# Optimization experiments

Hardware: AMD Instinct MI355X
Metric: run time of the kernel (lower is better)

Reference implementation:

```python
import jax, jax.numpy as jnp
import numpy as np

NUM_Q = 50000
DIM_KEY = 128
DIM_VALUE = 256
DIM_HIDDEN = 512
MEM_SIZE = 50
BATCH = 128
SEQ = 2048


def setup_inputs() -> dict:
    key = jax.random.key(0)
    ks = jax.random.split(key, 12)
    inp = {
        "q": jax.random.randint(ks[0], (BATCH, SEQ), 0, NUM_Q + 1, dtype=jnp.int64 if jax.config.jax_enable_x64 else jnp.int32),
        "a": jax.random.randint(ks[1], (BATCH, SEQ), 0, 2, dtype=jnp.int64 if jax.config.jax_enable_x64 else jnp.int32),
        # learned parameters (torch Linear convention: y = x @ W.T + b)
        "key_memory": jax.random.normal(ks[2], (MEM_SIZE, DIM_KEY), jnp.float32) * 0.1,
        "value_memory": jax.random.normal(ks[3], (MEM_SIZE, DIM_VALUE), jnp.float32) * 0.1,
        "embed_table": jax.random.normal(ks[4], (NUM_Q + 1, DIM_KEY), jnp.float32) * 0.1,
        "W_erase": jax.random.normal(ks[5], (DIM_VALUE, DIM_HIDDEN), jnp.float32) * 0.05,
        "b_erase": jnp.zeros((DIM_VALUE,), jnp.float32),
        "W_add": jax.random.normal(ks[6], (DIM_VALUE, DIM_HIDDEN), jnp.float32) * 0.05,
        "b_add": jnp.zeros((DIM_VALUE,), jnp.float32),
        "W_f": jax.random.normal(ks[7], (DIM_HIDDEN, DIM_VALUE + DIM_KEY), jnp.float32) * 0.05,
        "b_f": jnp.zeros((DIM_HIDDEN,), jnp.float32),
        "W_p": jax.random.normal(ks[8], (1, DIM_HIDDEN), jnp.float32) * 0.05,
        "b_p": jnp.zeros((1,), jnp.float32),
    }
    return inp


def reference(q, a, key_memory, value_memory, embed_table, W_erase, b_erase,
              W_add, b_add, W_f, b_f, W_p, b_p):
    # NOTE: in the original torch module, read() always uses the static
    # value_memory parameter (not the per-batch updated memory), and the
    # answer sequence `a` is never used in the forward math. Hence the
    # timestep loop is embarrassingly parallel and we vectorize over t.
    q_embed = embed_table[q]                                   # [B,S,K]
    corr = jax.nn.softmax(jnp.einsum('bsk,mk->bsm', q_embed, key_memory), axis=-1)  # [B,S,M]
    read_content = jnp.einsum('bsm,mv->bsv', corr, value_memory)                    # [B,S,V]
    feat = jnp.concatenate([read_content, q_embed], axis=-1)   # [B,S,V+K]
    # dropout is identity in eval mode
    state = jax.nn.relu(jnp.einsum('bsf,hf->bsh', feat, W_f) + b_f)                 # [B,S,H]
    pred = jax.nn.sigmoid(jnp.einsum('bsh,oh->bso', state, W_p) + b_p)              # [B,S,1]
    return pred[..., 0]                                        # [B,S]
```

## Files before the change

kernel.cpp:

```cpp
#include <hip/hip_runtime.h>
#include <hip/hip_bf16.h>

#define NUM_Q_MAX 50000
#define DIM_KEY 128
#define DIM_VAL 256
#define WF_COLS 384
#define DIM_HID 512
#define MEMN    50
#define KDIM    192
#define EOFF    56
#define PITCH   200
#define QB      64

typedef __bf16 bf16x8 __attribute__((ext_vector_type(8)));
typedef float  f32x4  __attribute__((ext_vector_type(4)));
union Frag { uint4 u; bf16x8 b; };

__device__ __forceinline__ float blo(unsigned u){ return __uint_as_float(u << 16); }
__device__ __forceinline__ float bhi(unsigned u){ return __uint_as_float(u & 0xffff0000u); }
__device__ __forceinline__ float b2f(unsigned short s){ return __uint_as_float(((unsigned)s) << 16); }
__device__ __forceinline__ unsigned short f2b(float x){
    unsigned u = __float_as_uint(x);
    u += 0x7fffu + ((u >> 16) & 1u);
    return (unsigned short)(u >> 16);
}

__global__ void prep_kernel(const float* __restrict__ Wf, const float* __restrict__ Vm,
                            unsigned short* __restrict__ WC){
    const int h = blockIdx.x;
    const int t = threadIdx.x;
    for (int j = t; j < KDIM; j += 64) {
        float val = 0.f;
        if (j < MEMN) {
            const float4* wr = (const float4*)(Wf + h * WF_COLS);
            const float4* vr = (const float4*)(Vm + j * DIM_VAL);
            float s = 0.f;
            for (int v = 0; v < DIM_VAL / 4; ++v) {
                float4 a = wr[v], b = vr[v];
                s += a.x*b.x + a.y*b.y + a.z*b.z + a.w*b.w;
            }
            val = s;
        } else if (j >= EOFF && j < EOFF + DIM_KEY) {
            val = Wf[h * WF_COLS + DIM_VAL + (j - EOFF)];
        }
        WC[h * KDIM + j] = f2b(val);
    }
}

__global__ void kb_kernel(const float* __restrict__ Kmem, unsigned short* __restrict__ Kb){
    int idx = blockIdx.x * 256 + threadIdx.x;
    if (idx < 64 * DIM_KEY) {
        int row = idx >> 7;
        float v = (row < MEMN) ? Kmem[idx] : 0.f;
        Kb[idx] = f2b(v);
    }
}

__global__ void __launch_bounds__(256)
table_kernel(const float* __restrict__ emb,
             const unsigned short* __restrict__ WC,
             const unsigned short* __restrict__ Kb,
             const float* __restrict__ bfv, const float* __restrict__ wpv,
             const float* __restrict__ bpv, float* __restrict__ table){
    __shared__ __align__(16) unsigned short xf[QB * PITCH];
    __shared__ float red[QB][4];
    const int tid  = threadIdx.x;
    const int u0   = blockIdx.x * QB;
    const int lane = tid & 63;
    const int wv   = tid >> 6;
    const int l15  = lane & 15;
    const int l4   = lane >> 4;

    #pragma unroll
    for (int n = 0; n < 4; ++n) {
        int c  = tid + 256 * n;
        int qi = c >> 4, c8 = c & 15;
        int u  = u0 + qi; if (u > NUM_Q_MAX) u = NUM_Q_MAX;
        const float4* src = (const float4*)(emb + (long)u * DIM_KEY + c8 * 8);
        float4 f0 = src[0], f1 = src[1];
        uint4 w;
        w.x = (unsigned)f2b(f0.x) | ((unsigned)f2b(f0.y) << 16);
        w.y = (unsigned)f2b(f0.z) | ((unsigned)f2b(f0.w) << 16);
        w.z = (unsigned)f2b(f1.x) | ((unsigned)f2b(f1.y) << 16);
        w.w = (unsigned)f2b(f1.z) | ((unsigned)f2b(f1.w) << 16);
        *(uint4*)&xf[qi * PITCH + EOFF + c8 * 8] = w;
    }
    if (tid < QB) {
        for (int j = MEMN; j < EOFF; ++j)              xf[tid * PITCH + j] = 0;
        for (int j = EOFF + DIM_KEY; j < PITCH; ++j)   xf[tid * PITCH + j] = 0;
    }
    __syncthreads();

    {
        Frag ef[4];
        #pragma unroll
        for (int ks = 0; ks < 4; ++ks)
            ef[ks].u = *(const uint4*)&xf[(wv*16 + l15) * PITCH + EOFF + ks*32 + l4*8];
        #pragma unroll
        for (int nt = 0; nt < 4; ++nt) {
            f32x4 acc = {0.f, 0.f, 0.f, 0.f};
            #pragma unroll
            for (int ks = 0; ks < 4; ++ks) {
                Frag bK;
                bK.u = *(const uint4*)&Kb[(nt*16 + l15) * DIM_KEY + ks*32 + l4*8];
                acc = __builtin_amdgcn_mfma_f32_16x16x32_bf16(ef[ks].b, bK.b, acc, 0, 0, 0);
            }
            int mcol = nt*16 + l15;
            if (mcol < MEMN) {
                #pragma unroll
                for (int r = 0; r < 4; ++r)
                    xf[(wv*16 + l4*4 + r) * PITCH + mcol] = f2b(acc[r]);
            }
        }
    }
    __syncthreads();

    if (tid < QB) {
        unsigned short* row = &xf[tid * PITCH];
        float mx = -1e30f;
        for (int m = 0; m < MEMN; ++m) mx = fmaxf(mx, b2f(row[m]));
        float sum = 0.f;
        for (int m = 0; m < MEMN; ++m) {
            float ev = __expf(b2f(row[m]) - mx);
            sum += ev;
            row[m] = f2b(ev);
        }
        float inv = 1.f / sum;
        for (int m = 0; m < MEMN; ++m) row[m] = f2b(b2f(row[m]) * inv);
    }
    __syncthreads();

    Frag af[4][6];
    #pragma unroll
    for (int m = 0; m < 4; ++m)
        #pragma unroll
        for (int ks = 0; ks < 6; ++ks)
            af[m][ks].u = *(const uint4*)&xf[(m*16 + l15) * PITCH + ks*32 + l4*8];

    float psum[4][4];
    #pragma unroll
    for (int m = 0; m < 4; ++m)
        #pragma unroll
        for (int r = 0; r < 4; ++r) psum[m][r] = 0.f;

    const int hbase = wv * 128;
    #pragma unroll
    for (int nt = 0; nt < 8; ++nt) {
        const int h0 = hbase + nt * 16;
        Frag bw[6];
        #pragma unroll
        for (int ks = 0; ks < 6; ++ks)
            bw[ks].u = *(const uint4*)&WC[(h0 + l15) * KDIM + ks*32 + l4*8];
        f32x4 acc[4];
        #pragma unroll
        for (int m = 0; m < 4; ++m) acc[m] = (f32x4){0.f, 0.f, 0.f, 0.f};
        #pragma unroll
        for (int ks = 0; ks < 6; ++ks)
            #pragma unroll
            for (int m = 0; m < 4; ++m)
                acc[m] = __builtin_amdgcn_mfma_f32_16x16x32_bf16(af[m][ks].b, bw[ks].b, acc[m], 0, 0, 0);
        const int h = h0 + l15;
        const float bb = bfv[h], ww = wpv[h];
        #pragma unroll
        for (int m = 0; m < 4; ++m)
            #pragma unroll
            for (int r = 0; r < 4; ++r) {
                float z = acc[m][r] + bb;
                if (z > 0.f) psum[m][r] += ww * z;
            }
    }

    #pragma unroll
    for (int off = 1; off < 16; off <<= 1)
        #pragma unroll
        for (int m = 0; m < 4; ++m)
            #pragma unroll
            for (int r = 0; r < 4; ++r)
                psum[m][r] += __shfl_xor(psum[m][r], off, 64);

    if (l15 == 0) {
        #pragma unroll
        for (int m = 0; m < 4; ++m)
            #pragma unroll
            for (int r = 0; r < 4; ++r)
                red[m*16 + l4*4 + r][wv] = psum[m][r];
    }
    __syncthreads();

    if (tid < QB) {
        float s = red[tid][0] + red[tid][1] + red[tid][2] + red[tid][3] + bpv[0];
        float p = 1.f / (1.f + __expf(-s));
        int u = u0 + tid;
        if (u <= NUM_Q_MAX) table[u] = p;
    }
}

__global__ void gather_kernel(const int* __restrict__ q, const float* __restrict__ table,
                              float* __restrict__ out, int n){
    int i = blockIdx.x * 256 + threadIdx.x;
    if (i < n) out[i] = table[q[i]];
}

extern "C" void kernel_launch(void* const* d_in, const int* in_sizes, int n_in,
                              void* d_out, int out_size, void* d_ws, size_t ws_size,
                              hipStream_t stream) {
    const int*   q    = (const int*)  d_in[0];
    const float* Kmem = (const float*)d_in[2];
    const float* Vmem = (const float*)d_in[3];
    const float* emb  = (const float*)d_in[4];
    const float* Wf   = (const float*)d_in[9];
    const float* bf   = (const float*)d_in[10];
    const float* wp   = (const float*)d_in[11];
    const float* bp   = (const float*)d_in[12];
    float* out = (float*)d_out;

    unsigned short* WC    = (unsigned short*)d_ws;
    unsigned short* Kb    = (unsigned short*)((char*)d_ws + 196608);
    float*          table = (float*)((char*)d_ws + 196608 + 16384);

    prep_kernel<<<DIM_HID, 64, 0, stream>>>(Wf, Vmem, WC);
    kb_kernel<<<32, 256, 0, stream>>>(Kmem, Kb);

    int nblk = (NUM_Q_MAX + 1 + QB - 1) / QB;
    table_kernel<<<nblk, 256, 0, stream>>>(emb, WC, Kb, bf, wp, bp, table);

    gather_kernel<<<(out_size + 255) / 256, 256, 0, stream>>>(q, table, out, out_size);
}
```

Measured before the change: 53.76 us.

## Restructure table kernel: 2x2 wave tiling, parallel softmax, double-buffered weight loads

Each wave now computes the key-score MFMA directly from embeddings loaded into registers, without round-tripping through LDS. Softmax is spread across all 256 threads, four per row, using shuffle reductions instead of 64 serial threads. The hidden GEMM is re-tiled so each wave covers 32 rows by 256 hidden units, double-buffering the WC fragment loads and prefetching the first tile and embedding-derived A fragments before the barrier. Launch bounds request 3 blocks per CU, which constrains registers. The aim is to hide global-load latency and cut serial softmax time, at the cost of higher register pressure and duplicate embedding loads.

```diff
diff --git a/kernel.cpp b/kernel.cpp
--- a/kernel.cpp
+++ b/kernel.cpp
@@ -18,11 +18,13 @@
 
 __device__ __forceinline__ float blo(unsigned u){ return __uint_as_float(u << 16); }
 __device__ __forceinline__ float bhi(unsigned u){ return __uint_as_float(u & 0xffff0000u); }
-__device__ __forceinline__ float b2f(unsigned short s){ return __uint_as_float(((unsigned)s) << 16); }
 __device__ __forceinline__ unsigned short f2b(float x){
     unsigned u = __float_as_uint(x);
     u += 0x7fffu + ((u >> 16) & 1u);
     return (unsigned short)(u >> 16);
+}
+__device__ __forceinline__ unsigned pk2(float a, float b){
+    return (unsigned)f2b(a) | ((unsigned)f2b(b) << 16);
 }
 
 __global__ void prep_kernel(const float* __restrict__ Wf, const float* __restrict__ Vm,
@@ -56,139 +58,186 @@
     }
 }
 
-__global__ void __launch_bounds__(256)
+__global__ void __launch_bounds__(256, 3)
 table_kernel(const float* __restrict__ emb,
              const unsigned short* __restrict__ WC,
              const unsigned short* __restrict__ Kb,
              const float* __restrict__ bfv, const float* __restrict__ wpv,
              const float* __restrict__ bpv, float* __restrict__ table){
     __shared__ __align__(16) unsigned short xf[QB * PITCH];
-    __shared__ float red[QB][4];
+    __shared__ float red[QB][2];
     const int tid  = threadIdx.x;
     const int u0   = blockIdx.x * QB;
     const int lane = tid & 63;
     const int wv   = tid >> 6;
     const int l15  = lane & 15;
     const int l4   = lane >> 4;
-
+    const int mg   = wv & 1;
+    const int hg   = wv >> 1;
+
+    float4 sg[4][2];
+    int sqi[4], sc8[4];
     #pragma unroll
     for (int n = 0; n < 4; ++n) {
         int c  = tid + 256 * n;
         int qi = c >> 4, c8 = c & 15;
         int u  = u0 + qi; if (u > NUM_Q_MAX) u = NUM_Q_MAX;
         const float4* src = (const float4*)(emb + (long)u * DIM_KEY + c8 * 8);
-        float4 f0 = src[0], f1 = src[1];
+        sg[n][0] = src[0]; sg[n][1] = src[1];
+        sqi[n] = qi; sc8[n] = c8;
+    }
+
+    int urow = u0 + wv * 16 + l15; if (urow > NUM_Q_MAX) urow = NUM_Q_MAX;
+    float4 eg[4][2];
+    #pragma unroll
+    for (int ks = 0; ks < 4; ++ks) {
+        const float4* src = (const float4*)(emb + (long)urow * DIM_KEY + ks * 32 + l4 * 8);
+        eg[ks][0] = src[0]; eg[ks][1] = src[1];
+    }
+
+    #pragma unroll
+    for (int n = 0; n < 4; ++n) {
         uint4 w;
-        w.x = (unsigned)f2b(f0.x) | ((unsigned)f2b(f0.y) << 16);
-        w.y = (unsigned)f2b(f0.z) | ((unsigned)f2b(f0.w) << 16);
-        w.z = (unsigned)f2b(f1.x) | ((unsigned)f2b(f1.y) << 16);
-        w.w = (unsigned)f2b(f1.z) | ((unsigned)f2b(f1.w) << 16);
-        *(uint4*)&xf[qi * PITCH + EOFF + c8 * 8] = w;
+        w.x = pk2(sg[n][0].x, sg[n][0].y); w.y = pk2(sg[n][0].z, sg[n][0].w);
+        w.z = pk2(sg[n][1].x, sg[n][1].y); w.w = pk2(sg[n][1].z, sg[n][1].w);
+        *(uint4*)&xf[sqi[n] * PITCH + EOFF + sc8[n] * 8] = w;
     }
     if (tid < QB) {
-        for (int j = MEMN; j < EOFF; ++j)              xf[tid * PITCH + j] = 0;
-        for (int j = EOFF + DIM_KEY; j < PITCH; ++j)   xf[tid * PITCH + j] = 0;
-    }
+        uint4 z = {0u, 0u, 0u, 0u};
+        *(uint4*)&xf[tid * PITCH + EOFF + DIM_KEY] = z;
+    }
+
+    Frag ef[4];
+    #pragma unroll
+    for (int ks = 0; ks < 4; ++ks) {
+        uint4 w;
+        w.x = pk2(eg[ks][0].x, eg[ks][0].y); w.y = pk2(eg[ks][0].z, eg[ks][0].w);
+        w.z = pk2(eg[ks][1].x, eg[ks][1].y); w.w = pk2(eg[ks][1].z, eg[ks][1].w);
+        ef[ks].u = w;
+    }
+    #pragma unroll
+    for (int nt = 0; nt < 4; ++nt) {
+        f32x4 acc = {0.f, 0.f, 0.f, 0.f};
+        #pragma unroll
+        for (int ks = 0; ks < 4; ++ks) {
+            Frag bk;
+            bk.u = *(const uint4*)&Kb[(nt*16 + l15) * DIM_KEY + ks*32 + l4*8];
+            acc = __builtin_amdgcn_mfma_f32_16x16x32_bf16(ef[ks].b, bk.b, acc, 0, 0, 0);
+        }
+        int mcol = nt*16 + l15;
+        if (mcol < MEMN) {
+            #pragma unroll
+            for (int r = 0; r < 4; ++r)
+                xf[(wv*16 + l4*4 + r) * PITCH + mcol] = f2b(acc[r]);
+        }
+    }
+
+    Frag bwA[6], bwB[6];
+    {
+        const int h0 = hg * 256;
+        #pragma unroll
+        for (int ks = 0; ks < 6; ++ks)
+            bwA[ks].u = *(const uint4*)&WC[(h0 + l15) * KDIM + ks*32 + l4*8];
+    }
+
     __syncthreads();
 
+    Frag af[2][6];
+    #pragma unroll
+    for (int mt = 0; mt < 2; ++mt)
+        #pragma unroll
+        for (int ks = 2; ks < 6; ++ks)
+            af[mt][ks].u = *(const uint4*)&xf[(mg*32 + mt*16 + l15) * PITCH + ks*32 + l4*8];
+
     {
-        Frag ef[4];
-        #pragma unroll
-        for (int ks = 0; ks < 4; ++ks)
-            ef[ks].u = *(const uint4*)&xf[(wv*16 + l15) * PITCH + EOFF + ks*32 + l4*8];
-        #pragma unroll
-        for (int nt = 0; nt < 4; ++nt) {
-            f32x4 acc = {0.f, 0.f, 0.f, 0.f};
-            #pragma unroll
-            for (int ks = 0; ks < 4; ++ks) {
-                Frag bK;
-                bK.u = *(const uint4*)&Kb[(nt*16 + l15) * DIM_KEY + ks*32 + l4*8];
-                acc = __builtin_amdgcn_mfma_f32_16x16x32_bf16(ef[ks].b, bK.b, acc, 0, 0, 0);
-            }
-            int mcol = nt*16 + l15;
-            if (mcol < MEMN) {
-                #pragma unroll
-                for (int r = 0; r < 4; ++r)
-                    xf[(wv*16 + l4*4 + r) * PITCH + mcol] = f2b(acc[r]);
-            }
+        const int r = tid >> 2, g = tid & 3;
+        unsigned short* rowp = &xf[r * PITCH];
+        uint4 v0 = *(const uint4*)&rowp[g * 16];
+        uint4 v1 = {0u, 0u, 0u, 0u};
+        if (g < 3) v1 = *(const uint4*)&rowp[g * 16 + 8];
+        float va[16];
+        va[0]=blo(v0.x); va[1]=bhi(v0.x); va[2]=blo(v0.y);  va[3]=bhi(v0.y);
+        va[4]=blo(v0.z); va[5]=bhi(v0.z); va[6]=blo(v0.w);  va[7]=bhi(v0.w);
+        va[8]=blo(v1.x); va[9]=bhi(v1.x); va[10]=blo(v1.y); va[11]=bhi(v1.y);
+        va[12]=blo(v1.z); va[13]=bhi(v1.z); va[14]=blo(v1.w); va[15]=bhi(v1.w);
+        const int c0 = g * 16;
+        float mx = -1e30f;
+        #pragma unroll
+        for (int e = 0; e < 16; ++e) if (c0 + e < MEMN) mx = fmaxf(mx, va[e]);
+        mx = fmaxf(mx, __shfl_xor(mx, 1, 64));
+        mx = fmaxf(mx, __shfl_xor(mx, 2, 64));
+        float sum = 0.f;
+        #pragma unroll
+        for (int e = 0; e < 16; ++e) {
+            float ev = (c0 + e < MEMN) ? __expf(va[e] - mx) : 0.f;
+            va[e] = ev; sum += ev;
+        }
+        sum += __shfl_xor(sum, 1, 64);
+        sum += __shfl_xor(sum, 2, 64);
+        const float inv = 1.f / sum;
+        uint4 w0, w1;
+        w0.x = pk2(va[0]*inv,  va[1]*inv);  w0.y = pk2(va[2]*inv,  va[3]*inv);
+        w0.z = pk2(va[4]*inv,  va[5]*inv);  w0.w = pk2(va[6]*inv,  va[7]*inv);
+        *(uint4*)&rowp[g * 16] = w0;
+        if (g < 3) {
+            w1.x = pk2(va[8]*inv,  va[9]*inv);  w1.y = pk2(va[10]*inv, va[11]*inv);
+            w1.z = pk2(va[12]*inv, va[13]*inv); w1.w = pk2(va[14]*inv, va[15]*inv);
+            *(uint4*)&rowp[g * 16 + 8] = w1;
         }
     }
     __syncthreads();
 
+    #pragma unroll
+    for (int mt = 0; mt < 2; ++mt)
+        #pragma unroll
+        for (int ks = 0; ks < 2; ++ks)
+            af[mt][ks].u = *(const uint4*)&xf[(mg*32 + mt*16 + l15) * PITCH + ks*32 + l4*8];
+
+    float psum[2][4] = {{0.f,0.f,0.f,0.f},{0.f,0.f,0.f,0.f}};
+    #pragma unroll
+    for (int nt = 0; nt < 16; ++nt) {
+        Frag* cur = (nt & 1) ? bwB : bwA;
+        Frag* nxt = (nt & 1) ? bwA : bwB;
+        if (nt < 15) {
+            const int h1 = hg * 256 + (nt + 1) * 16;
+            #pragma unroll
+            for (int ks = 0; ks < 6; ++ks)
+                nxt[ks].u = *(const uint4*)&WC[(h1 + l15) * KDIM + ks*32 + l4*8];
+        }
+        const int h = hg * 256 + nt * 16 + l15;
+        const float bb = bfv[h], ww = wpv[h];
+        f32x4 acc[2] = {{0.f,0.f,0.f,0.f},{0.f,0.f,0.f,0.f}};
+        #pragma unroll
+        for (int ks = 0; ks < 6; ++ks)
+            #pragma unroll
+            for (int mt = 0; mt < 2; ++mt)
+                acc[mt] = __builtin_amdgcn_mfma_f32_16x16x32_bf16(af[mt][ks].b, cur[ks].b, acc[mt], 0, 0, 0);
+        #pragma unroll
+        for (int mt = 0; mt < 2; ++mt)
+            #pragma unroll
+            for (int r = 0; r < 4; ++r)
+                psum[mt][r] += ww * fmaxf(acc[mt][r] + bb, 0.f);
+    }
+
+    #pragma unroll
+    for (int off = 1; off < 16; off <<= 1)
+        #pragma unroll
+        for (int mt = 0; mt < 2; ++mt)
+            #pragma unroll
+            for (int r = 0; r < 4; ++r)
+                psum[mt][r] += __shfl_xor(psum[mt][r], off, 64);
+
+    if (l15 == 0) {
+        #pragma unroll
+        for (int mt = 0; mt < 2; ++mt)
+            #pragma unroll
+            for (int r = 0; r < 4; ++r)
+                red[mg*32 + mt*16 + l4*4 + r][hg] = psum[mt][r];
+    }
+    __syncthreads();
+
     if (tid < QB) {
-        unsigned short* row = &xf[tid * PITCH];
-        float mx = -1e30f;
-        for (int m = 0; m < MEMN; ++m) mx = fmaxf(mx, b2f(row[m]));
-        float sum = 0.f;
-        for (int m = 0; m < MEMN; ++m) {
-            float ev = __expf(b2f(row[m]) - mx);
-            sum += ev;
-            row[m] = f2b(ev);
-        }
-        float inv = 1.f / sum;
-        for (int m = 0; m < MEMN; ++m) row[m] = f2b(b2f(row[m]) * inv);
-    }
-    __syncthreads();
-
-    Frag af[4][6];
-    #pragma unroll
-    for (int m = 0; m < 4; ++m)
-        #pragma unroll
-        for (int ks = 0; ks < 6; ++ks)
-            af[m][ks].u = *(const uint4*)&xf[(m*16 + l15) * PITCH + ks*32 + l4*8];
-
-    float psum[4][4];
-    #pragma unroll
-    for (int m = 0; m < 4; ++m)
-        #pragma unroll
-        for (int r = 0; r < 4; ++r) psum[m][r] = 0.f;
-
-    const int hbase = wv * 128;
-    #pragma unroll
-    for (int nt = 0; nt < 8; ++nt) {
-        const int h0 = hbase + nt * 16;
-        Frag bw[6];
-        #pragma unroll
-        for (int ks = 0; ks < 6; ++ks)
-            bw[ks].u = *(const uint4*)&WC[(h0 + l15) * KDIM + ks*32 + l4*8];
-        f32x4 acc[4];
-        #pragma unroll
-        for (int m = 0; m < 4; ++m) acc[m] = (f32x4){0.f, 0.f, 0.f, 0.f};
-        #pragma unroll
-        for (int ks = 0; ks < 6; ++ks)
-            #pragma unroll
-            for (int m = 0; m < 4; ++m)
-                acc[m] = __builtin_amdgcn_mfma_f32_16x16x32_bf16(af[m][ks].b, bw[ks].b, acc[m], 0, 0, 0);
-        const int h = h0 + l15;
-        const float bb = bfv[h], ww = wpv[h];
-        #pragma unroll
-        for (int m = 0; m < 4; ++m)
-            #pragma unroll
-            for (int r = 0; r < 4; ++r) {
-                float z = acc[m][r] + bb;
-                if (z > 0.f) psum[m][r] += ww * z;
-            }
-    }
-
-    #pragma unroll
-    for (int off = 1; off < 16; off <<= 1)
-        #pragma unroll
-        for (int m = 0; m < 4; ++m)
-            #pragma unroll
-            for (int r = 0; r < 4; ++r)
-                psum[m][r] += __shfl_xor(psum[m][r], off, 64);
-
-    if (l15 == 0) {
-        #pragma unroll
-        for (int m = 0; m < 4; ++m)
-            #pragma unroll
-            for (int r = 0; r < 4; ++r)
-                red[m*16 + l4*4 + r][wv] = psum[m][r];
-    }
-    __syncthreads();
-
-    if (tid < QB) {
-        float s = red[tid][0] + red[tid][1] + red[tid][2] + red[tid][3] + bpv[0];
+        float s = red[tid][0] + red[tid][1] + bpv[0];
         float p = 1.f / (1.f + __expf(-s));
         int u = u0 + tid;
         if (u <= NUM_Q_MAX) table[u] = p;
```

Measured after the change: 72.16 us. 34.2% more time.
